# Kernel tuning notes

Measured on AMD Instinct MI355X. Metric: run time of the kernel, lower is better.

Reference implementation:

```python
import jax, jax.numpy as jnp
import numpy as np
from jax.scipy.special import logsumexp

NUM_JOINT_TYPES = 17
SINKHORN_ITERS = 30
SINKHORN_TAU = 0.05
BIG_COST = 1.0e6


def _scot_forward(embeddings, W1, b1, prototype_pool, joint_types, k):
    n = embeddings.shape[0]
    # node encoder: Linear + SELU
    h = jax.nn.selu(embeddings @ W1 + b1)  # [N, H]
    prototypes = prototype_pool[:k]        # [K, H] (k <= k_max)
    # squared euclidean distance (torch.cdist(p=2).pow(2))
    d2 = (jnp.sum(h * h, axis=1)[:, None]
          + jnp.sum(prototypes * prototypes, axis=1)[None, :]
          - 2.0 * (h @ prototypes.T))
    d2 = jnp.maximum(d2, 0.0)              # [N, K]
    # expand each person slot to 17 joint-type slots
    cost = jnp.repeat(d2, NUM_JOINT_TYPES, axis=1)          # [N, K*17]
    slot_types = jnp.tile(jnp.arange(NUM_JOINT_TYPES), k)   # [K*17]
    type_mask = joint_types[:, None] == slot_types[None, :]  # [N, K*17]
    cost = jnp.where(type_mask, cost, BIG_COST)

    n_slots = k * NUM_JOINT_TYPES
    log_K = -cost / SINKHORN_TAU
    log_K_ext = jnp.concatenate([log_K, jnp.zeros((n, 1), log_K.dtype)], axis=1)  # [N, K*17+1]
    # target marginal: 1 per slot, slack column absorbs leftover mass
    tm = jnp.ones(n_slots + 1, log_K.dtype).at[-1].set(float(max(n - n_slots, 1)))
    log_tm = jnp.log(tm)

    def step(carry, _):
        log_u, log_v = carry
        log_u = -logsumexp(log_K_ext + log_v[None, :], axis=1)   # row normalization
        log_v = log_tm - logsumexp(log_K_ext + log_u[:, None], axis=0)  # col normalization
        return (log_u, log_v), None

    init = (jnp.zeros(n, log_K.dtype), jnp.zeros(n_slots + 1, log_K.dtype))
    (log_u, log_v), _ = jax.lax.scan(step, init, None, length=SINKHORN_ITERS)

    T = jnp.exp(log_K_ext + log_u[:, None] + log_v[None, :])[:, :n_slots]  # [N, K*17]
    logits = jnp.log(T.reshape(n, k, NUM_JOINT_TYPES).sum(axis=2) + 1e-8)  # [N, K]
    return logits, T


def setup_inputs() -> dict:
    key = jax.random.key(0)
    k_emb, k_w, k_proto, k_jt = jax.random.split(key, 4)
    N, D, H, KMAX = 6144, 256, 256, 512
    emb = jax.random.normal(k_emb, (N, D), dtype=jnp.float32)
    emb = emb / jnp.linalg.norm(emb, axis=1, keepdims=True)  # L2-normalised per docstring
    W1 = jax.random.normal(k_w, (D, H), dtype=jnp.float32) * (1.0 / np.sqrt(D))
    b1 = jnp.zeros((H,), jnp.float32)
    prototype_pool = jax.random.normal(k_proto, (KMAX, H), dtype=jnp.float32) * 0.5
    joint_types = jax.random.randint(k_jt, (N,), 0, NUM_JOINT_TYPES)
    return {"embeddings": emb, "W1": W1, "b1": b1,
            "prototype_pool": prototype_pool, "joint_types": joint_types, "k": 300}


def reference(embeddings, W1, b1, prototype_pool, joint_types, k):
    return _scot_forward(embeddings, W1, b1, prototype_pool, joint_types, k)
```

## Files before the change

kernel.cpp:

```cpp
#include <hip/hip_runtime.h>
#include <math.h>

#define NT 17
#define NB 34
#define KCAP 300
#define NITER 30
#define TR 4
#define MSCALE2 28.853900817779268f

typedef unsigned long long u64;
typedef float vfloat4 __attribute__((ext_vector_type(4)));

#define EX2(x) __builtin_amdgcn_exp2f(x)
#define LG2(x) __builtin_amdgcn_logf(x)
#if __has_builtin(__builtin_amdgcn_rcpf)
#define RCP(x) __builtin_amdgcn_rcpf(x)
#else
#define RCP(x) (1.0f / (x))
#endif


__device__ inline float selu_f(float x) {
  const float scale = 1.0507009873554804934193349852946f;
  const float alpha = 1.6732632423543772848170429916717f;
  return x > 0.f ? scale * x : scale * alpha * (EX2(x * 1.4426950408889634f) - 1.f);
}

__global__ __launch_bounds__(1024) void k_bucket(const int* __restrict__ jt, int n,
    int* __restrict__ meta, int* __restrict__ perm, int* __restrict__ tys) {
  __shared__ int hist[NT];
  __shared__ int off[NT];
  __shared__ int cnt[NT];
  int tid = threadIdx.x;
  if (tid < NT) { hist[tid] = 0; cnt[tid] = 0; }
  __syncthreads();
  for (int i = tid; i < n; i += 1024) atomicAdd(&hist[jt[i]], 1);
  __syncthreads();
  if (tid == 0) {
    int o = 0;
    for (int t = 0; t < NT; t++) {
      off[t] = o; meta[32 + t] = o; meta[t] = hist[t]; o += hist[t];
    }
  }
  __syncthreads();
  for (int i = tid; i < n; i += 1024) {
    int t = jt[i];
    int pos = off[t] + atomicAdd(&cnt[t], 1);
    perm[pos] = i;
    tys[pos] = t;
  }
}

__global__ __launch_bounds__(256) void k_hgemm(const float* __restrict__ A,
    const float* __restrict__ B, const float* __restrict__ bias,
    float* __restrict__ C, int n, int D, int H) {
  __shared__ __align__(16) float As[16][68];
  __shared__ __align__(16) float Bs[16][68];
  int tid = threadIdx.x;
  int i0 = blockIdx.x * 64, j0 = blockIdx.y * 64;
  int tx = tid & 15, ty = tid >> 4;
  int aI = tid & 63, aK = (tid >> 6) << 2;
  int bJ = (tid & 15) << 2, bK = tid >> 4;
  float acc[4][4] = {};
  for (int k0 = 0; k0 < D; k0 += 16) {
    float4 av = *(const float4*)(A + (size_t)(i0 + aI) * D + k0 + aK);
    float4 bv = *(const float4*)(B + (size_t)(k0 + bK) * H + j0 + bJ);
    __syncthreads();
    As[aK + 0][aI] = av.x; As[aK + 1][aI] = av.y; As[aK + 2][aI] = av.z; As[aK + 3][aI] = av.w;
    *(float4*)(&Bs[bK][bJ]) = bv;
    __syncthreads();
#pragma unroll
    for (int kk = 0; kk < 16; kk++) {
      float4 a4 = *(float4*)(&As[kk][ty << 2]);
      float4 b4 = *(float4*)(&Bs[kk][tx << 2]);
      float aa[4] = {a4.x, a4.y, a4.z, a4.w};
      float bb[4] = {b4.x, b4.y, b4.z, b4.w};
#pragma unroll
      for (int p = 0; p < 4; p++)
#pragma unroll
        for (int q = 0; q < 4; q++)
          acc[p][q] = fmaf(aa[p], bb[q], acc[p][q]);
    }
  }
#pragma unroll
  for (int p = 0; p < 4; p++) {
    int i = i0 + (ty << 2) + p;
    float o[4];
#pragma unroll
    for (int q = 0; q < 4; q++) {
      int j = j0 + (tx << 2) + q;
      o[q] = selu_f(acc[p][q] + bias[j]);
    }
    *(float4*)(C + (size_t)i * H + j0 + (tx << 2)) = make_float4(o[0], o[1], o[2], o[3]);
  }
}

__global__ __launch_bounds__(256) void k_msort(const float* __restrict__ h,
    const float* __restrict__ P, const int* __restrict__ perm,
    float* __restrict__ Ms, int n, int H, int k) {
  __shared__ __align__(16) float As[16][68];
  __shared__ __align__(16) float Bs[16][68];
  __shared__ float hp[4][64];
  __shared__ float pp[4][64];
  __shared__ int gIdx[64];
  int tid = threadIdx.x;
  int i0 = blockIdx.x * 64, j0 = blockIdx.y * 64;
  if (tid < 64) gIdx[tid] = perm[i0 + tid];
  __syncthreads();
  int tx = tid & 15, ty = tid >> 4;
  int aI = tid & 63, aK = (tid >> 6) << 2;
  int gA = gIdx[aI];
  bool bok = (j0 + aI) < k;
  const float* bRow = P + (size_t)(j0 + (bok ? aI : 0)) * H;
  float acc[4][4] = {};
  float ha = 0.f, pa = 0.f;
  for (int k0 = 0; k0 < H; k0 += 16) {
    float4 av = *(const float4*)(h + (size_t)gA * H + k0 + aK);
    float4 bv = *(const float4*)(bRow + k0 + aK);
    ha += av.x * av.x + av.y * av.y + av.z * av.z + av.w * av.w;
    pa += bv.x * bv.x + bv.y * bv.y + bv.z * bv.z + bv.w * bv.w;
    __syncthreads();
    As[aK + 0][aI] = av.x; As[aK + 1][aI] = av.y; As[aK + 2][aI] = av.z; As[aK + 3][aI] = av.w;
    Bs[aK + 0][aI] = bv.x; Bs[aK + 1][aI] = bv.y; Bs[aK + 2][aI] = bv.z; Bs[aK + 3][aI] = bv.w;
    __syncthreads();
#pragma unroll
    for (int kk = 0; kk < 16; kk++) {
      float4 a4 = *(float4*)(&As[kk][ty << 2]);
      float4 b4 = *(float4*)(&Bs[kk][tx << 2]);
      float aa[4] = {a4.x, a4.y, a4.z, a4.w};
      float bb[4] = {b4.x, b4.y, b4.z, b4.w};
#pragma unroll
      for (int p = 0; p < 4; p++)
#pragma unroll
        for (int q = 0; q < 4; q++)
          acc[p][q] = fmaf(aa[p], bb[q], acc[p][q]);
    }
  }
  int grp = tid >> 6;
  hp[grp][aI] = ha;
  pp[grp][aI] = pa;
  __syncthreads();
#pragma unroll
  for (int p = 0; p < 4; p++) {
    int rr = (ty << 2) + p;
    int r = i0 + rr;
    float hq = hp[0][rr] + hp[1][rr] + hp[2][rr] + hp[3][rr];
#pragma unroll
    for (int q = 0; q < 4; q++) {
      int jl = (tx << 2) + q;
      int j = j0 + jl;
      if (j < k) {
        float pq = pp[0][jl] + pp[1][jl] + pp[2][jl] + pp[3][jl];
        float d2 = hq + pq - 2.f * acc[p][q];
        d2 = fmaxf(d2, 0.f);
        Ms[(size_t)r * k + j] = -d2 * MSCALE2;
      }
    }
  }
}

__global__ __launch_bounds__(1024) void k_sink(float* __restrict__ Ms,
    const int* __restrict__ meta,
    float* __restrict__ cmD, unsigned* __restrict__ cmE,
    float* __restrict__ pcD, unsigned* __restrict__ pcE,
    float* __restrict__ suD, unsigned* __restrict__ suE,
    float* __restrict__ uF, float* __restrict__ vF,
    int k, float tm_last) {
  __shared__ __align__(16) float V[KCAP];
  __shared__ __align__(16) float Sown[KCAP];
  __shared__ __align__(16) float WP[16][304];
  __shared__ float uarr[512];
  __shared__ float SU[16];
  __shared__ float w_sh;
  __shared__ int lvl_ep;
  __shared__ int pairflag;
  int tid = threadIdx.x, lane = tid & 63, wv = tid >> 6;
  int c = blockIdx.x;
  int t = c >> 1, hb = c & 1, prt = c ^ 1;
  int cRt = meta[t];
  int s0t = meta[32 + t];
  int h0 = (cRt + 1) >> 1;
  int rb = hb ? h0 : 0;
  int re = hb ? cRt : h0;
  int myR = re - rb;
  int s0 = s0t + rb;
  int nt = (myR + TR - 1) / TR;
  bool l2v = (lane + 64) < (k >> 2);

  if (tid == 0) { pairflag = 0; w_sh = 1.f; lvl_ep = 0; }

  {
    float4 cm0 = make_float4(-3e38f, -3e38f, -3e38f, -3e38f);
    float4 cm1 = cm0;
    for (int tile = wv; tile < nt; tile += 16) {
      int r0 = tile * TR;
#pragma unroll
      for (int rr = 0; rr < TR; rr++) {
        int rc = (r0 + rr < myR) ? (r0 + rr) : r0;
        const float4* rp = (const float4*)(Ms + (size_t)(s0 + rc) * k);
        float4 a0 = rp[lane];
        cm0.x = fmaxf(cm0.x, a0.x); cm0.y = fmaxf(cm0.y, a0.y);
        cm0.z = fmaxf(cm0.z, a0.z); cm0.w = fmaxf(cm0.w, a0.w);
        if (l2v) {
          float4 a1 = rp[lane + 64];
          cm1.x = fmaxf(cm1.x, a1.x); cm1.y = fmaxf(cm1.y, a1.y);
          cm1.z = fmaxf(cm1.z, a1.z); cm1.w = fmaxf(cm1.w, a1.w);
        }
      }
    }
    *(float4*)&WP[wv][4 * lane] = cm0;
    if (l2v) *(float4*)&WP[wv][4 * (lane + 64)] = cm1;
    __syncthreads();
    if (tid < k) {
      float cmax = WP[0][tid];
#pragma unroll
      for (int q = 1; q < 16; q++) cmax = fmaxf(cmax, WP[q][tid]);
      Sown[tid] = cmax;
      __hip_atomic_store(&cmD[c * 304 + tid], cmax,
                         __ATOMIC_RELAXED, __HIP_MEMORY_SCOPE_AGENT);
    }
    __syncthreads();
    if (tid == 0) {
      __hip_atomic_store(&cmE[c * 16], 1u, __ATOMIC_RELAXED, __HIP_MEMORY_SCOPE_AGENT);
      while (__hip_atomic_load(&cmE[prt * 16], __ATOMIC_RELAXED, __HIP_MEMORY_SCOPE_AGENT) < 1u)
        __builtin_amdgcn_s_sleep(1);
      __hip_atomic_store(&pairflag, 1, __ATOMIC_RELEASE, __HIP_MEMORY_SCOPE_WORKGROUP);
    }
    if (tid < k) {
      while (__hip_atomic_load(&pairflag, __ATOMIC_ACQUIRE, __HIP_MEMORY_SCOPE_WORKGROUP) < 1)
        __builtin_amdgcn_s_sleep(1);
      float o = __hip_atomic_load(&cmD[prt * 304 + tid],
                                  __ATOMIC_RELAXED, __HIP_MEMORY_SCOPE_AGENT);
      V[tid] = fmaxf(Sown[tid], o);
    }
    __syncthreads();
    float4 c0 = *(const float4*)&V[4 * lane];
    float4 c1 = l2v ? *(const float4*)&V[4 * (lane + 64)] : c0;
    for (int tile = wv; tile < nt; tile += 16) {
      int r0 = tile * TR;
#pragma unroll
      for (int rr = 0; rr < TR; rr++) {
        int r = r0 + rr;
        if (r < myR) {
          float4* rp = (float4*)(Ms + (size_t)(s0 + r) * k);
          float4 a0 = rp[lane];
          a0.x = EX2(a0.x - c0.x); a0.y = EX2(a0.y - c0.y);
          a0.z = EX2(a0.z - c0.z); a0.w = EX2(a0.w - c0.w);
          rp[lane] = a0;
          if (l2v) {
            float4 a1 = rp[lane + 64];
            a1.x = EX2(a1.x - c1.x); a1.y = EX2(a1.y - c1.y);
            a1.z = EX2(a1.z - c1.z); a1.w = EX2(a1.w - c1.w);
            rp[lane + 64] = a1;
          }
        }
      }
    }
  }
  __syncthreads();
  if (tid < k) V[tid] = 0.f;
  __syncthreads();

  for (int m = 0; m < NITER; m++) {
    int epoch = m + 1;
    int slot = m & 3;
    if (wv == 15) {
      if (m > 0) {
        int pslot = (m - 1) & 3;
        unsigned want = (unsigned)m;
        bool need = lane < NB;
        for (;;) {
          bool ok = !need ||
              (__hip_atomic_load(&suE[(pslot * NB + lane) * 16],
                                 __ATOMIC_RELAXED, __HIP_MEMORY_SCOPE_AGENT) >= want);
          if (__all(ok)) break;
          __builtin_amdgcn_s_sleep(1);
        }
        float s = need
            ? __hip_atomic_load(&suD[(pslot * NB + lane) * 16],
                                __ATOMIC_RELAXED, __HIP_MEMORY_SCOPE_AGENT)
            : 0.f;
#pragma unroll
        for (int o = 32; o; o >>= 1) s += __shfl_xor(s, o);
        if (lane == 0) w_sh = tm_last / s;
      }
      if (lane == 0)
        __hip_atomic_store(&lvl_ep, epoch, __ATOMIC_RELEASE, __HIP_MEMORY_SCOPE_WORKGROUP);
    }
    float w = 0.f;
    bool haveW = (wv == 15);
    if (haveW) w = w_sh;
    float su = 0.f;
    float4 acc0 = make_float4(0.f, 0.f, 0.f, 0.f);
    float4 acc1 = acc0;
    float4 v0 = *(const float4*)&V[4 * lane];
    float4 v1 = l2v ? *(const float4*)&V[4 * (lane + 64)] : make_float4(0.f, 0.f, 0.f, 0.f);
    float4 a[TR][2], b[TR][2];

    auto loadTile = [&](int tile, float4 (&T)[TR][2]) {
      int r0 = tile * TR;
#pragma unroll
      for (int rr = 0; rr < TR; rr++) {
        int rc = (r0 + rr < myR) ? (r0 + rr) : r0;
        const float4* rp = (const float4*)(Ms + (size_t)(s0 + rc) * k);
        T[rr][0] = rp[lane];
        T[rr][1] = l2v ? rp[lane + 64] : make_float4(0.f, 0.f, 0.f, 0.f);
      }
    };
    auto computeTile = [&](int tile, float4 (&T)[TR][2]) {
      int r0 = tile * TR;
      float rs[TR];
#pragma unroll
      for (int rr = 0; rr < TR; rr++) {
        rs[rr] = T[rr][0].x * v0.x + T[rr][0].y * v0.y +
                 T[rr][0].z * v0.z + T[rr][0].w * v0.w +
                 T[rr][1].x * v1.x + T[rr][1].y * v1.y +
                 T[rr][1].z * v1.z + T[rr][1].w * v1.w;
      }
#pragma unroll
      for (int o = 32; o; o >>= 1) {
#pragma unroll
        for (int rr = 0; rr < TR; rr++) rs[rr] += __shfl_xor(rs[rr], o);
      }
      if (!haveW) {
        while (__hip_atomic_load(&lvl_ep, __ATOMIC_ACQUIRE, __HIP_MEMORY_SCOPE_WORKGROUP) < epoch)
          __builtin_amdgcn_s_sleep(1);
        w = w_sh;
        haveW = true;
      }
      float uu[TR];
#pragma unroll
      for (int rr = 0; rr < TR; rr++) {
        bool valid = (r0 + rr < myR);
        float u = RCP(rs[rr] + w);
        uu[rr] = valid ? u : 0.f;
        su += uu[rr];
        if (lane == 0 && valid) uarr[r0 + rr] = u;
      }
#pragma unroll
      for (int rr = 0; rr < TR; rr++) {
        acc0.x += T[rr][0].x * uu[rr]; acc0.y += T[rr][0].y * uu[rr];
        acc0.z += T[rr][0].z * uu[rr]; acc0.w += T[rr][0].w * uu[rr];
        acc1.x += T[rr][1].x * uu[rr]; acc1.y += T[rr][1].y * uu[rr];
        acc1.z += T[rr][1].z * uu[rr]; acc1.w += T[rr][1].w * uu[rr];
      }
    };

    int tile = wv;
    if (tile < nt) loadTile(tile, a);
    while (tile < nt) {
      int n1 = tile + 16;
      if (n1 < nt) loadTile(n1, b);
      computeTile(tile, a);
      if (n1 < nt) {
        int n2 = n1 + 16;
        if (n2 < nt) loadTile(n2, a);
        computeTile(n1, b);
      }
      tile += 32;
    }
    if (!haveW) {
      while (__hip_atomic_load(&lvl_ep, __ATOMIC_ACQUIRE, __HIP_MEMORY_SCOPE_WORKGROUP) < epoch)
        __builtin_amdgcn_s_sleep(1);
      haveW = true;
    }

    *(float4*)&WP[wv][4 * lane] = acc0;
    if (l2v) *(float4*)&WP[wv][4 * (lane + 64)] = acc1;
    if (lane == 0) SU[wv] = su;
    __syncthreads();
    if (tid < k) {
      float s = WP[0][tid];
#pragma unroll
      for (int q = 1; q < 16; q++) s += WP[q][tid];
      Sown[tid] = s;
      __hip_atomic_store(&pcD[(slot * NB + c) * 304 + tid], s,
                         __ATOMIC_RELAXED, __HIP_MEMORY_SCOPE_AGENT);
    }
    if (wv == 15) {
      float sp = (lane < 16) ? SU[lane] : 0.f;
#pragma unroll
      for (int o = 32; o; o >>= 1) sp += __shfl_xor(sp, o);
      if (lane == 0)
        __hip_atomic_store(&suD[(slot * NB + c) * 16], sp,
                           __ATOMIC_RELAXED, __HIP_MEMORY_SCOPE_AGENT);
      __builtin_amdgcn_s_waitcnt(0);
      if (lane == 0)
        __hip_atomic_store(&suE[(slot * NB + c) * 16], (unsigned)epoch,
                           __ATOMIC_RELAXED, __HIP_MEMORY_SCOPE_AGENT);
    }
    __syncthreads();
    if (tid == 0) {
      __hip_atomic_store(&pcE[(slot * NB + c) * 16], (unsigned)epoch,
                         __ATOMIC_RELAXED, __HIP_MEMORY_SCOPE_AGENT);
      while (__hip_atomic_load(&pcE[(slot * NB + prt) * 16],
                               __ATOMIC_RELAXED, __HIP_MEMORY_SCOPE_AGENT) < (unsigned)epoch)
        __builtin_amdgcn_s_sleep(1);
      __hip_atomic_store(&pairflag, m + 2, __ATOMIC_RELEASE, __HIP_MEMORY_SCOPE_WORKGROUP);
    }
    if (tid < k) {
      while (__hip_atomic_load(&pairflag, __ATOMIC_ACQUIRE, __HIP_MEMORY_SCOPE_WORKGROUP) < m + 2)
        __builtin_amdgcn_s_sleep(1);
      float sp = __hip_atomic_load(&pcD[(slot * NB + prt) * 304 + tid],
                                   __ATOMIC_RELAXED, __HIP_MEMORY_SCOPE_AGENT);
      V[tid] = RCP(Sown[tid] + sp);
    }
    __syncthreads();
  }
  for (int r = tid; r < myR; r += 1024) uF[s0 + r] = uarr[r];
  if (hb == 0)
    for (int j = tid; j < k; j += 1024) vF[(size_t)t * k + j] = V[j];
}

__global__ __launch_bounds__(256) void k_epi(const float* __restrict__ Ms,
    const float* __restrict__ uF, const float* __restrict__ vF,
    const int* __restrict__ perm, const int* __restrict__ tys,
    float* __restrict__ out, int n, int k) {
  __shared__ float vals[KCAP];
  int r = blockIdx.x;
  int i = perm[r], t = tys[r];
  float u = uF[r];
  const float* Krow = Ms + (size_t)r * k;
  const float* Vrow = vF + (size_t)t * k;
  for (int j = threadIdx.x; j < k; j += 256) vals[j] = Krow[j] * u * Vrow[j];
  __syncthreads();
  float* lg = out + (size_t)i * k;
  for (int j = threadIdx.x; j < k; j += 256)
    __builtin_nontemporal_store(LG2(vals[j] + 1e-8f) * 0.6931471805599453f, &lg[j]);
  int ns = k * NT;
  float* Trow = out + (size_t)n * k + (size_t)i * ns;
  if ((ns & 3) == 0) {
    int n4 = ns >> 2;
    int o0 = threadIdx.x << 2;
    int rmod = o0 % NT;
    for (int g4 = threadIdx.x; g4 < n4; g4 += 256, o0 += 1024) {
      int sstar = t - rmod; if (sstar < 0) sstar += NT;
      int j = (unsigned)(o0 + sstar) / (unsigned)NT;
      float vv = vals[j < k ? j : 0];
      vfloat4 v;
      v.x = (sstar == 0) ? vv : 0.f;
      v.y = (sstar == 1) ? vv : 0.f;
      v.z = (sstar == 2) ? vv : 0.f;
      v.w = (sstar == 3) ? vv : 0.f;
      __builtin_nontemporal_store(v, (vfloat4*)(Trow + o0));
      rmod += 4; if (rmod >= NT) rmod -= NT;
    }
  } else {
    for (int o = threadIdx.x; o < ns; o += 256) {
      int j = o / NT;
      int tt = o - j * NT;
      Trow[o] = (tt == t) ? vals[j] : 0.f;
    }
  }
}

extern "C" void kernel_launch(void* const* d_in, const int* in_sizes, int n_in,
                              void* d_out, int out_size, void* d_ws, size_t ws_size,
                              hipStream_t stream) {
  const float* emb = (const float*)d_in[0];
  const float* W1  = (const float*)d_in[1];
  const float* b1  = (const float*)d_in[2];
  const float* P   = (const float*)d_in[3];
  const int*   jt  = (const int*)d_in[4];
  (void)n_in; (void)ws_size;

  const int n = in_sizes[4];
  const int H = in_sizes[2];
  const int D = in_sizes[1] / H;
  const int k = out_size / (n * (NT + 1));
  const int nslots = k * NT;
  const float tm_last = (float)((n - nslots) > 1 ? (n - nslots) : 1);

  char* w = (char*)d_ws;
  size_t off = 0;
  auto take = [&](size_t bytes) -> char* {
    char* p = w + off;
    off = (off + bytes + 255) & ~(size_t)255;
    return p;
  };
  int*      meta = (int*)take(4096);
  int*      perm = (int*)take((size_t)n * 4);
  int*      tys  = (int*)take((size_t)n * 4);
  float*    h    = (float*)take((size_t)n * H * 4);
  float*    Ms   = (float*)take((size_t)n * k * 4);
  float*    cmD  = (float*)take((size_t)NB * 304 * 4);
  unsigned* cmE  = (unsigned*)take((size_t)NB * 64);
  float*    pcD  = (float*)take((size_t)4 * NB * 304 * 4);
  unsigned* pcE  = (unsigned*)take((size_t)4 * NB * 64);
  float*    suD  = (float*)take((size_t)4 * NB * 64);
  unsigned* suE  = (unsigned*)take((size_t)4 * NB * 64);
  float*    uF   = (float*)take((size_t)n * 4);
  float*    vF   = (float*)take((size_t)NT * k * 4);

  (void)hipMemsetAsync(cmE, 0, (size_t)NB * 64, stream);
  (void)hipMemsetAsync(pcE, 0, (size_t)4 * NB * 64, stream);
  (void)hipMemsetAsync(suE, 0, (size_t)4 * NB * 64, stream);
  k_bucket<<<1, 1024, 0, stream>>>(jt, n, meta, perm, tys);
  k_hgemm<<<dim3(n / 64, H / 64), dim3(256), 0, stream>>>(emb, W1, b1, h, n, D, H);
  k_msort<<<dim3(n / 64, (k + 63) / 64), dim3(256), 0, stream>>>(h, P, perm, Ms, n, H, k);
  k_sink<<<NB, 1024, 0, stream>>>(Ms, meta, cmD, cmE, pcD, pcE, suD, suE,
                                  uF, vF, k, tm_last);
  k_epi<<<n, 256, 0, stream>>>(Ms, uF, vF, perm, tys, (float*)d_out, n, k);
}
```

Baseline: 457.6 us.

## Use one workgroup per joint type in Sinkhorn, dropping pairwise cross-block exchange

The Sinkhorn kernel goes from two workgroups per joint type, which exchanged column maxima and partial column sums through global memory with spin-wait flags every iteration, to a single workgroup per type that owns all its rows. This removes the per-iteration pair handshake and its global atomics. Wave 15 is now dedicated to computing the slack weight w while the other 15 waves process row tiles. The cost is half as many active blocks (17 instead of 34), so each block streams about twice the rows and the number of CUs in use drops.

```diff
diff --git a/kernel.cpp b/kernel.cpp
--- a/kernel.cpp
+++ b/kernel.cpp
@@ -2,7 +2,7 @@
 #include <math.h>
 
 #define NT 17
-#define NB 34
+#define NB 17
 #define KCAP 300
 #define NITER 30
 #define TR 4
@@ -161,33 +161,23 @@
 
 __global__ __launch_bounds__(1024) void k_sink(float* __restrict__ Ms,
     const int* __restrict__ meta,
-    float* __restrict__ cmD, unsigned* __restrict__ cmE,
-    float* __restrict__ pcD, unsigned* __restrict__ pcE,
     float* __restrict__ suD, unsigned* __restrict__ suE,
     float* __restrict__ uF, float* __restrict__ vF,
     int k, float tm_last) {
   __shared__ __align__(16) float V[KCAP];
-  __shared__ __align__(16) float Sown[KCAP];
   __shared__ __align__(16) float WP[16][304];
-  __shared__ float uarr[512];
+  __shared__ float uarr[1024];
   __shared__ float SU[16];
   __shared__ float w_sh;
   __shared__ int lvl_ep;
-  __shared__ int pairflag;
   int tid = threadIdx.x, lane = tid & 63, wv = tid >> 6;
-  int c = blockIdx.x;
-  int t = c >> 1, hb = c & 1, prt = c ^ 1;
-  int cRt = meta[t];
-  int s0t = meta[32 + t];
-  int h0 = (cRt + 1) >> 1;
-  int rb = hb ? h0 : 0;
-  int re = hb ? cRt : h0;
-  int myR = re - rb;
-  int s0 = s0t + rb;
+  int t = blockIdx.x;
+  int myR = meta[t];
+  int s0 = meta[32 + t];
   int nt = (myR + TR - 1) / TR;
   bool l2v = (lane + 64) < (k >> 2);
 
-  if (tid == 0) { pairflag = 0; w_sh = 1.f; lvl_ep = 0; }
+  if (tid == 0) { w_sh = 1.f; lvl_ep = 0; }
 
   {
     float4 cm0 = make_float4(-3e38f, -3e38f, -3e38f, -3e38f);
@@ -215,23 +205,7 @@
       float cmax = WP[0][tid];
 #pragma unroll
       for (int q = 1; q < 16; q++) cmax = fmaxf(cmax, WP[q][tid]);
-      Sown[tid] = cmax;
-      __hip_atomic_store(&cmD[c * 304 + tid], cmax,
-                         __ATOMIC_RELAXED, __HIP_MEMORY_SCOPE_AGENT);
-    }
-    __syncthreads();
-    if (tid == 0) {
-      __hip_atomic_store(&cmE[c * 16], 1u, __ATOMIC_RELAXED, __HIP_MEMORY_SCOPE_AGENT);
-      while (__hip_atomic_load(&cmE[prt * 16], __ATOMIC_RELAXED, __HIP_MEMORY_SCOPE_AGENT) < 1u)
-        __builtin_amdgcn_s_sleep(1);
-      __hip_atomic_store(&pairflag, 1, __ATOMIC_RELEASE, __HIP_MEMORY_SCOPE_WORKGROUP);
-    }
-    if (tid < k) {
-      while (__hip_atomic_load(&pairflag, __ATOMIC_ACQUIRE, __HIP_MEMORY_SCOPE_WORKGROUP) < 1)
-        __builtin_amdgcn_s_sleep(1);
-      float o = __hip_atomic_load(&cmD[prt * 304 + tid],
-                                  __ATOMIC_RELAXED, __HIP_MEMORY_SCOPE_AGENT);
-      V[tid] = fmaxf(Sown[tid], o);
+      V[tid] = cmax;
     }
     __syncthreads();
     float4 c0 = *(const float4*)&V[4 * lane];
@@ -289,7 +263,6 @@
     }
     float w = 0.f;
     bool haveW = (wv == 15);
-    if (haveW) w = w_sh;
     float su = 0.f;
     float4 acc0 = make_float4(0.f, 0.f, 0.f, 0.f);
     float4 acc1 = acc0;
@@ -346,18 +319,18 @@
       }
     };
 
-    int tile = wv;
+    int tile = (wv < 15) ? wv : nt;
     if (tile < nt) loadTile(tile, a);
     while (tile < nt) {
-      int n1 = tile + 16;
+      int n1 = tile + 15;
       if (n1 < nt) loadTile(n1, b);
       computeTile(tile, a);
       if (n1 < nt) {
-        int n2 = n1 + 16;
+        int n2 = n1 + 15;
         if (n2 < nt) loadTile(n2, a);
         computeTile(n1, b);
       }
-      tile += 32;
+      tile += 30;
     }
     if (!haveW) {
       while (__hip_atomic_load(&lvl_ep, __ATOMIC_ACQUIRE, __HIP_MEMORY_SCOPE_WORKGROUP) < epoch)
@@ -373,43 +346,24 @@
       float s = WP[0][tid];
 #pragma unroll
       for (int q = 1; q < 16; q++) s += WP[q][tid];
-      Sown[tid] = s;
-      __hip_atomic_store(&pcD[(slot * NB + c) * 304 + tid], s,
-                         __ATOMIC_RELAXED, __HIP_MEMORY_SCOPE_AGENT);
+      V[tid] = RCP(s);
     }
     if (wv == 15) {
       float sp = (lane < 16) ? SU[lane] : 0.f;
 #pragma unroll
       for (int o = 32; o; o >>= 1) sp += __shfl_xor(sp, o);
       if (lane == 0)
-        __hip_atomic_store(&suD[(slot * NB + c) * 16], sp,
+        __hip_atomic_store(&suD[(slot * NB + t) * 16], sp,
                            __ATOMIC_RELAXED, __HIP_MEMORY_SCOPE_AGENT);
       __builtin_amdgcn_s_waitcnt(0);
       if (lane == 0)
-        __hip_atomic_store(&suE[(slot * NB + c) * 16], (unsigned)epoch,
+        __hip_atomic_store(&suE[(slot * NB + t) * 16], (unsigned)epoch,
                            __ATOMIC_RELAXED, __HIP_MEMORY_SCOPE_AGENT);
     }
     __syncthreads();
-    if (tid == 0) {
-      __hip_atomic_store(&pcE[(slot * NB + c) * 16], (unsigned)epoch,
-                         __ATOMIC_RELAXED, __HIP_MEMORY_SCOPE_AGENT);
-      while (__hip_atomic_load(&pcE[(slot * NB + prt) * 16],
-                               __ATOMIC_RELAXED, __HIP_MEMORY_SCOPE_AGENT) < (unsigned)epoch)
-        __builtin_amdgcn_s_sleep(1);
-      __hip_atomic_store(&pairflag, m + 2, __ATOMIC_RELEASE, __HIP_MEMORY_SCOPE_WORKGROUP);
-    }
-    if (tid < k) {
-      while (__hip_atomic_load(&pairflag, __ATOMIC_ACQUIRE, __HIP_MEMORY_SCOPE_WORKGROUP) < m + 2)
-        __builtin_amdgcn_s_sleep(1);
-      float sp = __hip_atomic_load(&pcD[(slot * NB + prt) * 304 + tid],
-                                   __ATOMIC_RELAXED, __HIP_MEMORY_SCOPE_AGENT);
-      V[tid] = RCP(Sown[tid] + sp);
-    }
-    __syncthreads();
   }
   for (int r = tid; r < myR; r += 1024) uF[s0 + r] = uarr[r];
-  if (hb == 0)
-    for (int j = tid; j < k; j += 1024) vF[(size_t)t * k + j] = V[j];
+  for (int j = tid; j < k; j += 1024) vF[(size_t)t * k + j] = V[j];
 }
 
 __global__ __launch_bounds__(256) void k_epi(const float* __restrict__ Ms,
@@ -483,22 +437,15 @@
   int*      tys  = (int*)take((size_t)n * 4);
   float*    h    = (float*)take((size_t)n * H * 4);
   float*    Ms   = (float*)take((size_t)n * k * 4);
-  float*    cmD  = (float*)take((size_t)NB * 304 * 4);
-  unsigned* cmE  = (unsigned*)take((size_t)NB * 64);
-  float*    pcD  = (float*)take((size_t)4 * NB * 304 * 4);
-  unsigned* pcE  = (unsigned*)take((size_t)4 * NB * 64);
   float*    suD  = (float*)take((size_t)4 * NB * 64);
   unsigned* suE  = (unsigned*)take((size_t)4 * NB * 64);
   float*    uF   = (float*)take((size_t)n * 4);
   float*    vF   = (float*)take((size_t)NT * k * 4);
 
-  (void)hipMemsetAsync(cmE, 0, (size_t)NB * 64, stream);
-  (void)hipMemsetAsync(pcE, 0, (size_t)4 * NB * 64, stream);
   (void)hipMemsetAsync(suE, 0, (size_t)4 * NB * 64, stream);
   k_bucket<<<1, 1024, 0, stream>>>(jt, n, meta, perm, tys);
   k_hgemm<<<dim3(n / 64, H / 64), dim3(256), 0, stream>>>(emb, W1, b1, h, n, D, H);
   k_msort<<<dim3(n / 64, (k + 63) / 64), dim3(256), 0, stream>>>(h, P, perm, Ms, n, H, k);
-  k_sink<<<NB, 1024, 0, stream>>>(Ms, meta, cmD, cmE, pcD, pcE, suD, suE,
-                                  uF, vF, k, tm_last);
+  k_sink<<<NB, 1024, 0, stream>>>(Ms, meta, suD, suE, uF, vF, k, tm_last);
   k_epi<<<n, 256, 0, stream>>>(Ms, uF, vF, perm, tys, (float*)d_out, n, k);
 }
```

Measured after the change: 550.1 us. +20.2%, slower.
